# Optimization experiments

Hardware: AMD Instinct MI355X
Metric: run time of the kernel (lower is better)

## Reference

```python
import jax, jax.numpy as jnp
import numpy as np

WIN = 8          # window side -> N = 64 tokens per window
HEADS = 8
NCAV = 2
EGO_DIST_BINS = 4
EGO_ANGLE_BINS = 4


def _rel_pos_index(wh, ww):
    # Swin-style relative position index, (wh*ww, wh*ww) int
    coords = np.stack(np.meshgrid(np.arange(wh), np.arange(ww), indexing='ij'))  # (2,wh,ww)
    flat = coords.reshape(2, -1)
    rel = (flat[:, :, None] - flat[:, None, :]).transpose(1, 2, 0).astype(np.int64)
    rel[:, :, 0] += wh - 1
    rel[:, :, 1] += ww - 1
    rel[:, :, 0] *= 2 * ww - 1
    return jnp.asarray(rel.sum(-1))


def _ego_bias_index(affine_matrix, H, W):
    # per-(cav,window) bin index into ego_position_bias_table
    gy, gx = jnp.meshgrid(jnp.arange(H // WIN), jnp.arange(W // WIN), indexing='ij')
    centers = jnp.stack([gx * WIN + WIN / 2.0, gy * WIN + WIN / 2.0], axis=-1)
    centers = centers.reshape(-1, 2).astype(jnp.float32)              # (nW, 2)
    img_c = jnp.array([[W / 2.0], [H / 2.0]], jnp.float32)            # (2, 1)
    ego = (affine_matrix[:, :2, :2] @ img_c + affine_matrix[:, :2, 2:3])[..., 0]  # (ncav, 2)
    rel = centers[None, :, :] - ego[:, None, :]                        # (ncav, nW, 2)
    dist = jnp.linalg.norm(rel, axis=-1)
    ang = jnp.arctan2(rel[..., 1], rel[..., 0])
    db = (dist / (dist.max() + 1e-6) * (EGO_DIST_BINS - 1)).astype(jnp.int32)
    ab = ((ang + jnp.pi) / (2 * jnp.pi) * (EGO_ANGLE_BINS - 1)).astype(jnp.int32)
    return (db * EGO_ANGLE_BINS + ab).reshape(-1)                      # (ncav*nW,) == (B_,)


def setup_inputs() -> dict:
    key = jax.random.key(0)
    ks = jax.random.split(key, 10)
    H = W = 256
    B_ = NCAV * (H // WIN) * (W // WIN)   # 2048
    N = WIN * WIN                          # 64
    C = 256
    s = 0.02
    return {
        'x': jax.random.normal(ks[0], (B_, N, C), jnp.float32),
        'affine_matrix': jax.random.normal(ks[1], (NCAV, 2, 3), jnp.float32),
        'Wq': jax.random.normal(ks[2], (C, C), jnp.float32) * s,
        'bq': jax.random.normal(ks[3], (C,), jnp.float32) * s,
        'Wkv': jax.random.normal(ks[4], (C, 2 * C), jnp.float32) * s,
        'bkv': jax.random.normal(ks[5], (2 * C,), jnp.float32) * s,
        'Wp': jax.random.normal(ks[6], (C, C), jnp.float32) * s,
        'bp': jax.random.normal(ks[7], (C,), jnp.float32) * s,
        'rel_table': jax.random.normal(ks[8], ((2 * WIN - 1) ** 2, HEADS), jnp.float32) * s,
        'ego_table': jax.random.normal(ks[9], (EGO_DIST_BINS * EGO_ANGLE_BINS, HEADS), jnp.float32) * s,
        'w': jnp.ones((2,), jnp.float32),
        'H': H,
        'W': W,
    }


def reference(x, affine_matrix, Wq, bq, Wkv, bkv, Wp, bp, rel_table, ego_table, w, H, W):
    B_, N, C = x.shape
    h = HEADS
    hd = C // h
    scale = hd ** -0.5

    q = (x @ Wq + bq).reshape(B_, N, h, hd).transpose(0, 2, 1, 3)          # (B_, h, N, hd)
    kv = (x @ Wkv + bkv).reshape(B_, N, 2, h, hd).transpose(2, 0, 3, 1, 4)
    k, v = kv[0], kv[1]                                                     # (B_, h, N, hd)

    attn = jnp.einsum('bhnd,bhmd->bhnm', q * scale, k)                      # (B_, h, N, N)

    # Swin relative position bias
    rpi = _rel_pos_index(WIN, WIN)
    rel_bias = rel_table[rpi.reshape(-1)].reshape(N, N, h).transpose(2, 0, 1)  # (h, N, N)

    # ego-relative bias: one scalar per (window, head), broadcast over NxN
    idx = _ego_bias_index(affine_matrix, H, W)                              # (B_,)
    ego_bias = ego_table[idx]                                               # (B_, h)

    attn = attn + rel_bias[None, :, :, :] + ego_bias[:, :, None, None]

    attn0 = jax.nn.softmax(attn, axis=-1)
    attn1 = jnp.square(jnp.maximum(attn, 0.0))   # relu(attn)**2 (no-mask branch)
    ws = jax.nn.softmax(w)
    attn = attn0 * ws[0] + attn1 * ws[1]

    out = jnp.einsum('bhnm,bhmd->bhnd', attn, v).transpose(0, 2, 1, 3).reshape(B_, N, C)
    return out @ Wp + bp
```

## Files before the change

### kernel.cpp

```cpp
#include <hip/hip_runtime.h>

#define NWIN 2048
#define NT   64
#define CDIM 256
#define NHEAD 8
#define HD   32
#define SCALE 0.17677669529663687f

typedef short bfrag __attribute__((ext_vector_type(8)));
typedef float f4    __attribute__((ext_vector_type(4)));
typedef unsigned short us4 __attribute__((ext_vector_type(4)));

__device__ __forceinline__ unsigned short f2bf(float f){
  unsigned u = __builtin_bit_cast(unsigned, f);
  u += 0x7FFFu + ((u >> 16) & 1u);
  return (unsigned short)(u >> 16);
}

__device__ __forceinline__ f4 mfma16(bfrag a, bfrag b, f4 c){
  return __builtin_amdgcn_mfma_f32_16x16x32_bf16(a, b, c, 0, 0, 0);
}

__global__ void prep_kernel(const float* __restrict__ aff,
                            const float* __restrict__ Wq,  const float* __restrict__ bq,
                            const float* __restrict__ Wkv, const float* __restrict__ bkv,
                            const float* __restrict__ Wp,
                            const float* __restrict__ relt, const float* __restrict__ egot,
                            unsigned short* __restrict__ wt, float* __restrict__ relb,
                            float* __restrict__ egob, float* __restrict__ bqkv)
{
  const int bid = blockIdx.x, tid = threadIdx.x;
  if (bid < 1024) {
    int r = bid, c = tid;
    float v;
    if (r < 256)      v = Wq[c*256 + r] * SCALE;
    else if (r < 768) v = Wkv[c*512 + (r - 256)];
    else              v = Wp[c*256 + (r - 768)];
    wt[r*256 + c] = f2bf(v);
  } else if (bid < 1152) {
    int e = (bid - 1024)*256 + tid;
    int h = e >> 12, i = (e >> 6) & 63, j = e & 63;
    int yi = i >> 3, xi = i & 7, yj = j >> 3, xj = j & 7;
    int ridx = (yi - yj + 7)*15 + (xi - xj + 7);
    relb[e] = relt[ridx*8 + h];
  } else if (bid == 1152) {
    __shared__ float red[256];
    float ex[2], ey[2];
    for (int cv = 0; cv < 2; ++cv){
      const float* A = aff + cv*6;
      ex[cv] = (A[0] + A[1])*128.0f + A[2];
      ey[cv] = (A[3] + A[4])*128.0f + A[5];
    }
    float dl = 0.0f;
    for (int p = 0; p < 4; ++p){
      int t = p*256 + tid;
      float cx = (float)((t & 31)*8 + 4), cy = (float)((t >> 5)*8 + 4);
      for (int cv = 0; cv < 2; ++cv){
        float dx = cx - ex[cv], dy = cy - ey[cv];
        dl = fmaxf(dl, sqrtf(dx*dx + dy*dy));
      }
    }
    red[tid] = dl; __syncthreads();
    for (int s = 128; s > 0; s >>= 1){
      if (tid < s) red[tid] = fmaxf(red[tid], red[tid + s]);
      __syncthreads();
    }
    float dmax = red[0] + 1e-6f;
    const float PI_F = 3.14159265358979f;
    for (int p = 0; p < 4; ++p){
      int t = p*256 + tid;
      float cx = (float)((t & 31)*8 + 4), cy = (float)((t >> 5)*8 + 4);
      for (int cv = 0; cv < 2; ++cv){
        float dx = cx - ex[cv], dy = cy - ey[cv];
        float d = sqrtf(dx*dx + dy*dy);
        float ang = atan2f(dy, dx);
        int db = (int)(d / dmax * 3.0f);
        int ab = (int)((ang + PI_F) / (2.0f*PI_F) * 3.0f);
        int idx = db*4 + ab;
        int bw = cv*1024 + t;
        for (int h2 = 0; h2 < 8; ++h2)
          egob[bw*8 + h2] = egot[idx*8 + h2];
      }
    }
  } else {
    for (int j = tid; j < 768; j += 256)
      bqkv[j] = (j < 256) ? bq[j]*SCALE : bkv[j - 256];
  }
}

__global__ __launch_bounds__(1024) void attn_kernel(
    const float* __restrict__ x, const float* __restrict__ wvec,
    const float* __restrict__ bp, float* __restrict__ out,
    const unsigned short* __restrict__ wt, const float* __restrict__ relb,
    const float* __restrict__ egob, const float* __restrict__ bqkv)
{
  __shared__ unsigned short lds_x[NT*CDIM];
  __shared__ unsigned short lds_qkv[NHEAD*6144];

  const int b = blockIdx.x;
  const int tid = threadIdx.x;
  const int wv = tid >> 6, lane = tid & 63;
  const int quad = lane >> 4, cc = lane & 15;

  const float4* xg = (const float4*)(x + (size_t)b*(NT*CDIM));
  for (int it = 0; it < 4; ++it){
    int i4 = tid + it*1024;
    float4 v = xg[i4];
    us4 pk = { f2bf(v.x), f2bf(v.y), f2bf(v.z), f2bf(v.w) };
    *(us4*)(&lds_x[i4*4]) = pk;
  }
  float w0 = wvec[0], w1 = wvec[1];
  float wm = fmaxf(w0, w1);
  float e0 = __expf(w0 - wm), e1 = __expf(w1 - wm);
  float ws0 = e0/(e0+e1), ws1 = e1/(e0+e1);
  __syncthreads();

  {
    const int ob = wv*48;
    f4 acc[3][4];
    for (int mt=0;mt<3;++mt) for (int nt=0;nt<4;++nt) acc[mt][nt] = (f4){0,0,0,0};
    for (int ks = 0; ks < 8; ++ks){
      bfrag afr[3], bfr[4];
      for (int mt=0;mt<3;++mt)
        afr[mt] = *(const bfrag*)(wt + (ob + mt*16 + cc)*256 + ks*32 + quad*8);
      for (int nt=0;nt<4;++nt)
        bfr[nt] = *(const bfrag*)(&lds_x[(nt*16 + cc)*256 + ks*32 + quad*8]);
      for (int mt=0;mt<3;++mt)
        for (int nt=0;nt<4;++nt)
          acc[mt][nt] = mfma16(afr[mt], bfr[nt], acc[mt][nt]);
    }
    for (int mt=0;mt<3;++mt){
      int oc0 = ob + mt*16 + quad*4;
      float bb0 = bqkv[oc0], bb1 = bqkv[oc0+1], bb2 = bqkv[oc0+2], bb3 = bqkv[oc0+3];
      int part = oc0 >> 8, ch = oc0 & 255;
      int h2 = ch >> 5, d0 = ch & 31;
      unsigned short* slab = &lds_qkv[h2*6144 + part*2048];
      for (int nt=0;nt<4;++nt){
        int tok = nt*16 + cc;
        float v0 = acc[mt][nt][0] + bb0;
        float v1 = acc[mt][nt][1] + bb1;
        float v2 = acc[mt][nt][2] + bb2;
        float v3 = acc[mt][nt][3] + bb3;
        if (part < 2){
          us4 pk = { f2bf(v0), f2bf(v1), f2bf(v2), f2bf(v3) };
          *(us4*)(&slab[tok*32 + d0]) = pk;
        } else {
          slab[(d0+0)*64 + tok] = f2bf(v0);
          slab[(d0+1)*64 + tok] = f2bf(v1);
          slab[(d0+2)*64 + tok] = f2bf(v2);
          slab[(d0+3)*64 + tok] = f2bf(v3);
        }
      }
    }
  }
  __syncthreads();

  const int h = wv >> 1, half = wv & 1;
  f4 yacc[2][2];
  {
    const unsigned short* qs  = &lds_qkv[h*6144];
    const unsigned short* ks_ = qs + 2048;
    const unsigned short* vts = qs + 4096;
    float ego = egob[b*8 + h];
    const float* rb = relb + h*4096;

    bfrag bk[4];
    for (int jt=0;jt<4;++jt)
      bk[jt] = *(const bfrag*)(&ks_[(jt*16 + cc)*32 + quad*8]);
    f4 S[2][4];
    for (int it=0;it<2;++it){
      bfrag aq = *(const bfrag*)(&qs[(half*32 + it*16 + cc)*32 + quad*8]);
      for (int jt=0;jt<4;++jt){
        f4 z = (f4){0,0,0,0};
        S[it][jt] = mfma16(aq, bk[jt], z);
      }
    }
    float a[2][4][4];
    for (int it=0;it<2;++it)
      for (int jt=0;jt<4;++jt){
        int jj = jt*16 + cc;
        for (int r=0;r<4;++r){
          int ii = half*32 + it*16 + quad*4 + r;
          a[it][r][jt] = S[it][jt][r] + rb[ii*64 + jj] + ego;
        }
      }
    float rmax[2][4], rinv[2][4];
    for (int it=0;it<2;++it)
      for (int r=0;r<4;++r){
        float m = fmaxf(fmaxf(a[it][r][0], a[it][r][1]), fmaxf(a[it][r][2], a[it][r][3]));
        for (int off=1; off<16; off<<=1) m = fmaxf(m, __shfl_xor(m, off, 64));
        float s = 0.0f;
        for (int jt=0;jt<4;++jt) s += __expf(a[it][r][jt] - m);
        for (int off=1; off<16; off<<=1) s += __shfl_xor(s, off, 64);
        rmax[it][r] = m; rinv[it][r] = 1.0f / s;
      }
    for (int it=0;it<2;++it) for (int nt=0;nt<2;++nt) yacc[it][nt] = (f4){0,0,0,0};
    unsigned short* Pw = &lds_x[wv*1024];
    for (int chunk=0; chunk<2; ++chunk){
      for (int it=0;it<2;++it)
        for (int jtl=0;jtl<2;++jtl){
          int jt = chunk*2 + jtl;
          for (int r=0;r<4;++r){
            float av = a[it][r][jt];
            float rl = fmaxf(av, 0.0f);
            float p = ws0 * __expf(av - rmax[it][r]) * rinv[it][r] + ws1 * rl * rl;
            Pw[(it*16 + quad*4 + r)*32 + jtl*16 + cc] = f2bf(p);
          }
        }
      bfrag pa[2], pb[2];
      for (int itl=0;itl<2;++itl)
        pa[itl] = *(const bfrag*)(&Pw[(itl*16 + cc)*32 + quad*8]);
      for (int nt=0;nt<2;++nt)
        pb[nt] = *(const bfrag*)(&vts[(nt*16 + cc)*64 + chunk*32 + quad*8]);
      for (int itl=0;itl<2;++itl)
        for (int nt=0;nt<2;++nt)
          yacc[itl][nt] = mfma16(pa[itl], pb[nt], yacc[itl][nt]);
    }
  }
  __syncthreads();
  for (int itl=0;itl<2;++itl)
    for (int nt=0;nt<2;++nt)
      for (int r=0;r<4;++r){
        int ii = half*32 + itl*16 + quad*4 + r;
        lds_x[ii*256 + h*32 + nt*16 + cc] = f2bf(yacc[itl][nt][r]);
      }
  __syncthreads();

  {
    const int mt = wv & 3;
    const int cb = (wv >> 2)*64;
    f4 o[4];
    for (int nt=0;nt<4;++nt) o[nt] = (f4){0,0,0,0};
    for (int ks=0; ks<8; ++ks){
      bfrag ay = *(const bfrag*)(&lds_x[(mt*16 + cc)*256 + ks*32 + quad*8]);
      for (int nt=0;nt<4;++nt){
        bfrag bw = *(const bfrag*)(wt + (768 + cb + nt*16 + cc)*256 + ks*32 + quad*8);
        o[nt] = mfma16(ay, bw, o[nt]);
      }
    }
    float* og = out + (size_t)b*(NT*CDIM);
    for (int nt=0;nt<4;++nt){
      int col = cb + nt*16 + cc;
      float bpv = bp[col];
      for (int r=0;r<4;++r){
        int tok = mt*16 + quad*4 + r;
        og[tok*256 + col] = o[nt][r] + bpv;
      }
    }
  }
}

extern "C" void kernel_launch(void* const* d_in, const int* in_sizes, int n_in,
                              void* d_out, int out_size, void* d_ws, size_t ws_size,
                              hipStream_t stream)
{
  const float* x    = (const float*)d_in[0];
  const float* aff  = (const float*)d_in[1];
  const float* Wq   = (const float*)d_in[2];
  const float* bq   = (const float*)d_in[3];
  const float* Wkv  = (const float*)d_in[4];
  const float* bkv  = (const float*)d_in[5];
  const float* Wp   = (const float*)d_in[6];
  const float* bp   = (const float*)d_in[7];
  const float* relt = (const float*)d_in[8];
  const float* egot = (const float*)d_in[9];
  const float* w    = (const float*)d_in[10];
  float* out = (float*)d_out;

  char* ws = (char*)d_ws;
  unsigned short* wt = (unsigned short*)ws;
  float* relb = (float*)(ws + 524288);
  float* egob = (float*)(ws + 655360);
  float* bqkv = (float*)(ws + 720896);

  hipLaunchKernelGGL(prep_kernel, dim3(1154), dim3(256), 0, stream,
                     aff, Wq, bq, Wkv, bkv, Wp, relt, egot, wt, relb, egob, bqkv);
  hipLaunchKernelGGL(attn_kernel, dim3(2048), dim3(1024), 0, stream,
                     x, w, bp, out, wt, relb, egob, bqkv);
}
```

Baseline: 512.6 us.

## Persistent attention blocks with x prefetch, padded LDS layouts, tiled weight transpose

The attention kernel now runs 256 persistent blocks that each process 8 windows. The next window's x is prefetched into registers while the current one is computed, and bias and projection constants are hoisted out of the per-window loop. LDS rows for x, Q/K and V^T are padded to cut bank conflicts, and the rel-bias table is stored transposed so it can be read as a vector. The prep kernel transposes the weights through a shared-memory tile for coalesced access. The trade-off is that only 256 blocks fill the GPU, plus extra barriers and higher register pressure.

```diff
diff --git a/kernel.cpp b/kernel.cpp
--- a/kernel.cpp
+++ b/kernel.cpp
@@ -4,8 +4,12 @@
 #define NT   64
 #define CDIM 256
 #define NHEAD 8
-#define HD   32
 #define SCALE 0.17677669529663687f
+
+#define XP 264
+#define QP 40
+#define VP 72
+#define HSLAB 7424
 
 typedef short bfrag __attribute__((ext_vector_type(8)));
 typedef float f4    __attribute__((ext_vector_type(4)));
@@ -30,20 +34,36 @@
                             float* __restrict__ egob, float* __restrict__ bqkv)
 {
   const int bid = blockIdx.x, tid = threadIdx.x;
-  if (bid < 1024) {
-    int r = bid, c = tid;
-    float v;
-    if (r < 256)      v = Wq[c*256 + r] * SCALE;
-    else if (r < 768) v = Wkv[c*512 + (r - 256)];
-    else              v = Wp[c*256 + (r - 768)];
-    wt[r*256 + c] = f2bf(v);
-  } else if (bid < 1152) {
-    int e = (bid - 1024)*256 + tid;
-    int h = e >> 12, i = (e >> 6) & 63, j = e & 63;
-    int yi = i >> 3, xi = i & 7, yj = j >> 3, xj = j & 7;
-    int ridx = (yi - yj + 7)*15 + (xi - xj + 7);
-    relb[e] = relt[ridx*8 + h];
-  } else if (bid == 1152) {
+  if (bid < 64) {
+    __shared__ float tile[64][65];
+    int R  = (bid >> 2) * 64;
+    int Cb = (bid & 3) * 64;
+    for (int t = 0; t < 16; ++t){
+      int idx = t*256 + tid;
+      int cl = idx >> 6, rl = idx & 63;
+      int r = R + rl, c = Cb + cl;
+      float v;
+      if (r < 256)      v = Wq[c*256 + r] * SCALE;
+      else if (r < 768) v = Wkv[c*512 + (r - 256)];
+      else              v = Wp[c*256 + (r - 768)];
+      tile[cl][rl] = v;
+    }
+    __syncthreads();
+    for (int t = 0; t < 16; ++t){
+      int idx = t*256 + tid;
+      int rl = idx >> 6, cl = idx & 63;
+      wt[(R + rl)*256 + Cb + cl] = f2bf(tile[cl][rl]);
+    }
+  } else if (bid < 96) {
+    int e0 = (bid - 64)*1024 + tid*4;
+    for (int u = 0; u < 4; ++u){
+      int e = e0 + u;
+      int h = e >> 12, j = (e >> 6) & 63, i = e & 63;
+      int yi = i >> 3, xi = i & 7, yj = j >> 3, xj = j & 7;
+      int ridx = (yi - yj + 7)*15 + (xi - xj + 7);
+      relb[e] = relt[ridx*8 + h];
+    }
+  } else if (bid == 96) {
     __shared__ float red[256];
     float ex[2], ey[2];
     for (int cv = 0; cv < 2; ++cv){
@@ -94,159 +114,214 @@
     const unsigned short* __restrict__ wt, const float* __restrict__ relb,
     const float* __restrict__ egob, const float* __restrict__ bqkv)
 {
-  __shared__ unsigned short lds_x[NT*CDIM];
-  __shared__ unsigned short lds_qkv[NHEAD*6144];
-
-  const int b = blockIdx.x;
+  __shared__ unsigned short lds_x[20480];
+  __shared__ unsigned short lds_qkv[NHEAD*HSLAB];
+
   const int tid = threadIdx.x;
   const int wv = tid >> 6, lane = tid & 63;
   const int quad = lane >> 4, cc = lane & 15;
-
-  const float4* xg = (const float4*)(x + (size_t)b*(NT*CDIM));
-  for (int it = 0; it < 4; ++it){
-    int i4 = tid + it*1024;
-    float4 v = xg[i4];
-    us4 pk = { f2bf(v.x), f2bf(v.y), f2bf(v.z), f2bf(v.w) };
-    *(us4*)(&lds_x[i4*4]) = pk;
-  }
+  const int h = wv >> 1, half = wv & 1;
+
   float w0 = wvec[0], w1 = wvec[1];
   float wm = fmaxf(w0, w1);
   float e0 = __expf(w0 - wm), e1 = __expf(w1 - wm);
   float ws0 = e0/(e0+e1), ws1 = e1/(e0+e1);
-  __syncthreads();
-
-  {
-    const int ob = wv*48;
-    f4 acc[3][4];
-    for (int mt=0;mt<3;++mt) for (int nt=0;nt<4;++nt) acc[mt][nt] = (f4){0,0,0,0};
-    for (int ks = 0; ks < 8; ++ks){
-      bfrag afr[3], bfr[4];
+
+  const int ob = wv*48;
+  float bb[3][4];
+  #pragma unroll
+  for (int mt=0;mt<3;++mt){
+    int oc0 = ob + mt*16 + quad*4;
+    #pragma unroll
+    for (int r2=0;r2<4;++r2) bb[mt][r2] = bqkv[oc0+r2];
+  }
+  const int mt3 = wv & 3, cbase = (wv >> 2)*64;
+  float bpv[4];
+  #pragma unroll
+  for (int nt=0;nt<4;++nt) bpv[nt] = bp[cbase + nt*16 + cc];
+
+  int wid = blockIdx.x * 8;
+  const float4* xg = (const float4*)x;
+  float4 xp[4];
+  #pragma unroll
+  for (int k=0;k<4;++k) xp[k] = xg[(size_t)wid*4096 + tid + k*1024];
+
+  for (int i = 0; i < 8; ++i, ++wid){
+    #pragma unroll
+    for (int k=0;k<4;++k){
+      int i4 = tid + k*1024;
+      int row = i4 >> 6, c4 = i4 & 63;
+      float4 v = xp[k];
+      us4 pk = { f2bf(v.x), f2bf(v.y), f2bf(v.z), f2bf(v.w) };
+      *(us4*)(&lds_x[row*XP + c4*4]) = pk;
+    }
+    if (i < 7){
+      #pragma unroll
+      for (int k=0;k<4;++k) xp[k] = xg[(size_t)(wid+1)*4096 + tid + k*1024];
+    }
+    __syncthreads();
+
+    {
+      f4 acc[3][4];
+      #pragma unroll
       for (int mt=0;mt<3;++mt)
-        afr[mt] = *(const bfrag*)(wt + (ob + mt*16 + cc)*256 + ks*32 + quad*8);
-      for (int nt=0;nt<4;++nt)
-        bfr[nt] = *(const bfrag*)(&lds_x[(nt*16 + cc)*256 + ks*32 + quad*8]);
-      for (int mt=0;mt<3;++mt)
+        #pragma unroll
+        for (int nt=0;nt<4;++nt) acc[mt][nt] = (f4){0,0,0,0};
+      #pragma unroll
+      for (int ks = 0; ks < 8; ++ks){
+        bfrag afr[3], bfr[4];
+        #pragma unroll
+        for (int mt=0;mt<3;++mt)
+          afr[mt] = *(const bfrag*)(wt + (ob + mt*16 + cc)*256 + ks*32 + quad*8);
+        #pragma unroll
         for (int nt=0;nt<4;++nt)
-          acc[mt][nt] = mfma16(afr[mt], bfr[nt], acc[mt][nt]);
-    }
-    for (int mt=0;mt<3;++mt){
-      int oc0 = ob + mt*16 + quad*4;
-      float bb0 = bqkv[oc0], bb1 = bqkv[oc0+1], bb2 = bqkv[oc0+2], bb3 = bqkv[oc0+3];
-      int part = oc0 >> 8, ch = oc0 & 255;
-      int h2 = ch >> 5, d0 = ch & 31;
-      unsigned short* slab = &lds_qkv[h2*6144 + part*2048];
+          bfr[nt] = *(const bfrag*)(&lds_x[(nt*16 + cc)*XP + ks*32 + quad*8]);
+        #pragma unroll
+        for (int mt=0;mt<3;++mt)
+          #pragma unroll
+          for (int nt=0;nt<4;++nt)
+            acc[mt][nt] = mfma16(afr[mt], bfr[nt], acc[mt][nt]);
+      }
+      #pragma unroll
+      for (int mt=0;mt<3;++mt){
+        int oc0 = ob + mt*16 + quad*4;
+        int part = oc0 >> 8, ch = oc0 & 255;
+        int h2 = ch >> 5, d0 = ch & 31;
+        #pragma unroll
+        for (int nt=0;nt<4;++nt){
+          int tok = nt*16 + cc;
+          float v0 = acc[mt][nt][0] + bb[mt][0];
+          float v1 = acc[mt][nt][1] + bb[mt][1];
+          float v2 = acc[mt][nt][2] + bb[mt][2];
+          float v3 = acc[mt][nt][3] + bb[mt][3];
+          if (part < 2){
+            unsigned short* sl = &lds_qkv[h2*HSLAB + part*2560];
+            us4 pk = { f2bf(v0), f2bf(v1), f2bf(v2), f2bf(v3) };
+            *(us4*)(&sl[tok*QP + d0]) = pk;
+          } else {
+            unsigned short* vt = &lds_qkv[h2*HSLAB + 5120];
+            vt[(d0+0)*VP + tok] = f2bf(v0);
+            vt[(d0+1)*VP + tok] = f2bf(v1);
+            vt[(d0+2)*VP + tok] = f2bf(v2);
+            vt[(d0+3)*VP + tok] = f2bf(v3);
+          }
+        }
+      }
+    }
+    __syncthreads();
+
+    f4 yacc[2][2];
+    {
+      const unsigned short* qs  = &lds_qkv[h*HSLAB];
+      const unsigned short* ks_ = qs + 2560;
+      const unsigned short* vts = qs + 5120;
+      float ego = egob[wid*8 + h];
+      const float* rbh = relb + h*4096;
+
+      bfrag bk[4];
+      #pragma unroll
+      for (int jt=0;jt<4;++jt)
+        bk[jt] = *(const bfrag*)(&ks_[(jt*16 + cc)*QP + quad*8]);
+
+      f4 a4[2][4];
+      #pragma unroll
+      for (int it=0;it<2;++it){
+        bfrag aq = *(const bfrag*)(&qs[(half*32 + it*16 + cc)*QP + quad*8]);
+        #pragma unroll
+        for (int jt=0;jt<4;++jt){
+          f4 z = (f4){0,0,0,0};
+          f4 S = mfma16(aq, bk[jt], z);
+          f4 rb = *(const f4*)(&rbh[(jt*16 + cc)*64 + half*32 + it*16 + quad*4]);
+          a4[it][jt] = S + rb + ego;
+        }
+      }
+      float rmax[2][4], rinv[2][4];
+      #pragma unroll
+      for (int it=0;it<2;++it)
+        #pragma unroll
+        for (int r=0;r<4;++r){
+          float m = fmaxf(fmaxf(a4[it][0][r], a4[it][1][r]),
+                          fmaxf(a4[it][2][r], a4[it][3][r]));
+          #pragma unroll
+          for (int off=1; off<16; off<<=1) m = fmaxf(m, __shfl_xor(m, off, 64));
+          float s = __expf(a4[it][0][r]-m) + __expf(a4[it][1][r]-m)
+                  + __expf(a4[it][2][r]-m) + __expf(a4[it][3][r]-m);
+          #pragma unroll
+          for (int off=1; off<16; off<<=1) s += __shfl_xor(s, off, 64);
+          rmax[it][r] = m; rinv[it][r] = ws0 / s;
+        }
+      #pragma unroll
+      for (int it=0;it<2;++it)
+        #pragma unroll
+        for (int nt=0;nt<2;++nt) yacc[it][nt] = (f4){0,0,0,0};
+      unsigned short* Pw = &lds_x[wv*1280];
+      #pragma unroll
+      for (int chunk=0; chunk<2; ++chunk){
+        #pragma unroll
+        for (int it=0;it<2;++it)
+          #pragma unroll
+          for (int jtl=0;jtl<2;++jtl){
+            int jt = chunk*2 + jtl;
+            #pragma unroll
+            for (int r=0;r<4;++r){
+              float av = a4[it][jt][r];
+              float rl = fmaxf(av, 0.0f);
+              float p = rinv[it][r]*__expf(av - rmax[it][r]) + ws1*rl*rl;
+              Pw[(it*16 + quad*4 + r)*QP + jtl*16 + cc] = f2bf(p);
+            }
+          }
+        bfrag pa[2], pb[2];
+        #pragma unroll
+        for (int itl=0;itl<2;++itl)
+          pa[itl] = *(const bfrag*)(&Pw[(itl*16 + cc)*QP + quad*8]);
+        #pragma unroll
+        for (int nt=0;nt<2;++nt)
+          pb[nt] = *(const bfrag*)(&vts[(nt*16 + cc)*VP + chunk*32 + quad*8]);
+        #pragma unroll
+        for (int itl=0;itl<2;++itl)
+          #pragma unroll
+          for (int nt=0;nt<2;++nt)
+            yacc[itl][nt] = mfma16(pa[itl], pb[nt], yacc[itl][nt]);
+      }
+    }
+    __syncthreads();
+
+    #pragma unroll
+    for (int itl=0;itl<2;++itl)
+      #pragma unroll
+      for (int nt=0;nt<2;++nt)
+        #pragma unroll
+        for (int r=0;r<4;++r){
+          int ii = half*32 + itl*16 + quad*4 + r;
+          lds_x[ii*XP + h*32 + nt*16 + cc] = f2bf(yacc[itl][nt][r]);
+        }
+    __syncthreads();
+
+    {
+      f4 o[4];
+      #pragma unroll
+      for (int nt=0;nt<4;++nt) o[nt] = (f4){0,0,0,0};
+      #pragma unroll
+      for (int ks=0; ks<8; ++ks){
+        bfrag ay = *(const bfrag*)(&lds_x[(mt3*16 + cc)*XP + ks*32 + quad*8]);
+        #pragma unroll
+        for (int nt=0;nt<4;++nt){
+          bfrag bw = *(const bfrag*)(wt + (768 + cbase + nt*16 + cc)*256 + ks*32 + quad*8);
+          o[nt] = mfma16(ay, bw, o[nt]);
+        }
+      }
+      float* og = out + (size_t)wid*(NT*CDIM);
+      #pragma unroll
       for (int nt=0;nt<4;++nt){
-        int tok = nt*16 + cc;
-        float v0 = acc[mt][nt][0] + bb0;
-        float v1 = acc[mt][nt][1] + bb1;
-        float v2 = acc[mt][nt][2] + bb2;
-        float v3 = acc[mt][nt][3] + bb3;
-        if (part < 2){
-          us4 pk = { f2bf(v0), f2bf(v1), f2bf(v2), f2bf(v3) };
-          *(us4*)(&slab[tok*32 + d0]) = pk;
-        } else {
-          slab[(d0+0)*64 + tok] = f2bf(v0);
-          slab[(d0+1)*64 + tok] = f2bf(v1);
-          slab[(d0+2)*64 + tok] = f2bf(v2);
-          slab[(d0+3)*64 + tok] = f2bf(v3);
-        }
-      }
-    }
-  }
-  __syncthreads();
-
-  const int h = wv >> 1, half = wv & 1;
-  f4 yacc[2][2];
-  {
-    const unsigned short* qs  = &lds_qkv[h*6144];
-    const unsigned short* ks_ = qs + 2048;
-    const unsigned short* vts = qs + 4096;
-    float ego = egob[b*8 + h];
-    const float* rb = relb + h*4096;
-
-    bfrag bk[4];
-    for (int jt=0;jt<4;++jt)
-      bk[jt] = *(const bfrag*)(&ks_[(jt*16 + cc)*32 + quad*8]);
-    f4 S[2][4];
-    for (int it=0;it<2;++it){
-      bfrag aq = *(const bfrag*)(&qs[(half*32 + it*16 + cc)*32 + quad*8]);
-      for (int jt=0;jt<4;++jt){
-        f4 z = (f4){0,0,0,0};
-        S[it][jt] = mfma16(aq, bk[jt], z);
-      }
-    }
-    float a[2][4][4];
-    for (int it=0;it<2;++it)
-      for (int jt=0;jt<4;++jt){
-        int jj = jt*16 + cc;
+        int col = cbase + nt*16 + cc;
+        #pragma unroll
         for (int r=0;r<4;++r){
-          int ii = half*32 + it*16 + quad*4 + r;
-          a[it][r][jt] = S[it][jt][r] + rb[ii*64 + jj] + ego;
-        }
-      }
-    float rmax[2][4], rinv[2][4];
-    for (int it=0;it<2;++it)
-      for (int r=0;r<4;++r){
-        float m = fmaxf(fmaxf(a[it][r][0], a[it][r][1]), fmaxf(a[it][r][2], a[it][r][3]));
-        for (int off=1; off<16; off<<=1) m = fmaxf(m, __shfl_xor(m, off, 64));
-        float s = 0.0f;
-        for (int jt=0;jt<4;++jt) s += __expf(a[it][r][jt] - m);
-        for (int off=1; off<16; off<<=1) s += __shfl_xor(s, off, 64);
-        rmax[it][r] = m; rinv[it][r] = 1.0f / s;
-      }
-    for (int it=0;it<2;++it) for (int nt=0;nt<2;++nt) yacc[it][nt] = (f4){0,0,0,0};
-    unsigned short* Pw = &lds_x[wv*1024];
-    for (int chunk=0; chunk<2; ++chunk){
-      for (int it=0;it<2;++it)
-        for (int jtl=0;jtl<2;++jtl){
-          int jt = chunk*2 + jtl;
-          for (int r=0;r<4;++r){
-            float av = a[it][r][jt];
-            float rl = fmaxf(av, 0.0f);
-            float p = ws0 * __expf(av - rmax[it][r]) * rinv[it][r] + ws1 * rl * rl;
-            Pw[(it*16 + quad*4 + r)*32 + jtl*16 + cc] = f2bf(p);
-          }
-        }
-      bfrag pa[2], pb[2];
-      for (int itl=0;itl<2;++itl)
-        pa[itl] = *(const bfrag*)(&Pw[(itl*16 + cc)*32 + quad*8]);
-      for (int nt=0;nt<2;++nt)
-        pb[nt] = *(const bfrag*)(&vts[(nt*16 + cc)*64 + chunk*32 + quad*8]);
-      for (int itl=0;itl<2;++itl)
-        for (int nt=0;nt<2;++nt)
-          yacc[itl][nt] = mfma16(pa[itl], pb[nt], yacc[itl][nt]);
-    }
-  }
-  __syncthreads();
-  for (int itl=0;itl<2;++itl)
-    for (int nt=0;nt<2;++nt)
-      for (int r=0;r<4;++r){
-        int ii = half*32 + itl*16 + quad*4 + r;
-        lds_x[ii*256 + h*32 + nt*16 + cc] = f2bf(yacc[itl][nt][r]);
-      }
-  __syncthreads();
-
-  {
-    const int mt = wv & 3;
-    const int cb = (wv >> 2)*64;
-    f4 o[4];
-    for (int nt=0;nt<4;++nt) o[nt] = (f4){0,0,0,0};
-    for (int ks=0; ks<8; ++ks){
-      bfrag ay = *(const bfrag*)(&lds_x[(mt*16 + cc)*256 + ks*32 + quad*8]);
-      for (int nt=0;nt<4;++nt){
-        bfrag bw = *(const bfrag*)(wt + (768 + cb + nt*16 + cc)*256 + ks*32 + quad*8);
-        o[nt] = mfma16(ay, bw, o[nt]);
-      }
-    }
-    float* og = out + (size_t)b*(NT*CDIM);
-    for (int nt=0;nt<4;++nt){
-      int col = cb + nt*16 + cc;
-      float bpv = bp[col];
-      for (int r=0;r<4;++r){
-        int tok = mt*16 + quad*4 + r;
-        og[tok*256 + col] = o[nt][r] + bpv;
-      }
-    }
+          int tok = mt3*16 + quad*4 + r;
+          og[tok*256 + col] = o[nt][r] + bpv[nt];
+        }
+      }
+    }
+    __syncthreads();
   }
 }
 
@@ -273,8 +348,8 @@
   float* egob = (float*)(ws + 655360);
   float* bqkv = (float*)(ws + 720896);
 
-  hipLaunchKernelGGL(prep_kernel, dim3(1154), dim3(256), 0, stream,
+  hipLaunchKernelGGL(prep_kernel, dim3(98), dim3(256), 0, stream,
                      aff, Wq, bq, Wkv, bkv, Wp, relt, egot, wt, relb, egob, bqkv);
-  hipLaunchKernelGGL(attn_kernel, dim3(2048), dim3(1024), 0, stream,
+  hipLaunchKernelGGL(attn_kernel, dim3(256), dim3(1024), 0, stream,
                      x, w, bp, out, wt, relb, egob, bqkv);
 }
```

Result: slower. 808.6 us (+57.8%).
